# Performance work log

Measured on AMD Instinct MI355X. Metric: run time of the kernel, lower is better.

Reference implementation:

```python
import jax, jax.numpy as jnp
import numpy as np

N = 100000        # num nodes
F_IN = 256        # params['topo_feature']
C = 128           # params['num_edge'] (hidden & GCN channels)
E = 1_600_000     # num edges (avg degree 16)


def setup_inputs() -> dict:
    key = jax.random.key(0)
    k = jax.random.split(key, 6)
    x = jax.random.normal(k[0], (N, F_IN), dtype=jnp.float32)
    edge_index = jax.random.randint(k[1], (2, E), 0, N, dtype=jnp.int32)
    # fc1: Linear(F_IN, C)
    W1 = jax.random.normal(k[2], (C, F_IN), dtype=jnp.float32) * (1.0 / np.sqrt(F_IN))
    b1 = jnp.zeros((C,), dtype=jnp.float32)
    # GCNConv linear: Linear(C, C, bias=False) weight + separate bias added post-aggregation
    W2 = jax.random.normal(k[3], (C, C), dtype=jnp.float32) * (1.0 / np.sqrt(C))
    b2 = jnp.zeros((C,), dtype=jnp.float32)
    return {"x": x, "edge_index": edge_index, "W1": W1, "b1": b1, "W2": W2, "b2": b2}


def reference(x, edge_index, W1, b1, W2, b2):
    # fc1 + relu
    h = jax.nn.relu(x @ W1.T + b1)                       # [N, C]
    # GCNConv: transform, add self-loops, sym-normalize, scatter-add
    z = h @ W2.T                                         # [N, C]
    loop = jnp.arange(N, dtype=edge_index.dtype)
    src = jnp.concatenate([edge_index[0], loop])         # [E+N]
    dst = jnp.concatenate([edge_index[1], loop])         # [E+N]
    deg = jax.ops.segment_sum(jnp.ones_like(dst, jnp.float32), dst, num_segments=N)
    dinv = jnp.where(deg > 0, jax.lax.rsqrt(jnp.maximum(deg, 1.0)), 0.0)
    norm = (dinv[src] * dinv[dst])[:, None]              # [E+N, 1]
    out = jax.ops.segment_sum(z[src] * norm, dst, num_segments=N) + b2
    return out
```

## Files before the change

kernel.cpp:

```cpp
#include <hip/hip_runtime.h>

typedef unsigned short ushort;
typedef __bf16 bf16x8 __attribute__((ext_vector_type(8)));
typedef float f32x4 __attribute__((ext_vector_type(4)));

#define F_IN 256
#define CCH  128
#define BSH  7
#define BNODES 128
#define NBUCK 1024
#define CHUNK 2048

__device__ __forceinline__ ushort f2bf(float f) {
    union { float f; unsigned i; } u; u.f = f;
    unsigned r = u.i + 0x7fffu + ((u.i >> 16) & 1u);
    return (ushort)(r >> 16);
}
__device__ __forceinline__ float2 bf2f2(unsigned u) {
    union { unsigned i; float f; } lo, hi;
    lo.i = u << 16;
    hi.i = u & 0xffff0000u;
    return make_float2(lo.f, hi.f);
}
__device__ __forceinline__ void gload_lds16(const void* g, void* l) {
    __builtin_amdgcn_global_load_lds((const __attribute__((address_space(1))) unsigned*)g,
                                     (__attribute__((address_space(3))) unsigned*)l, 16, 0, 0);
}

__global__ __launch_bounds__(256)
void hist_cvt(const int* __restrict__ dst, int* __restrict__ histC, int* __restrict__ histT,
              int E, int nchunks, int ncp,
              const float* __restrict__ W1, const float* __restrict__ W2,
              ushort* __restrict__ w1b, ushort* __restrict__ w2b)
{
    const int blk = blockIdx.x, t = threadIdx.x;
    if (blk >= nchunks) {
        int i = (blk - nchunks) * 256 + t;
        if (i < CCH * F_IN) {
            int c  = i & 31;
            int cs = c ^ (((i >> 9) & 3) << 3);
            w1b[(i & ~31) | cs] = f2bf(W1[i]);
        } else {
            int j = i - CCH * F_IN;
            if (j < CCH * CCH) w2b[j] = f2bf(W2[j]);
        }
        return;
    }
    __shared__ int h[NBUCK];
    for (int i = t; i < NBUCK; i += 256) h[i] = 0;
    __syncthreads();
    int cb = blk * CHUNK, ce = min(cb + CHUNK, E);
    for (int e = cb + t; e < ce; e += 256)
        atomicAdd(&h[dst[e] >> BSH], 1);
    __syncthreads();
    const int ncp16 = ncp * 16;
    for (int i = t; i < NBUCK; i += 256) {
        int v = h[i];
        histC[blk * NBUCK + i] = v;
        histT[(i >> 4) * ncp16 + blk * 16 + (i & 15)] = v;
    }
}

__global__ __launch_bounds__(1024)
void scan_buckets(int* __restrict__ histT, int* __restrict__ btot, int nchunks, int ncp)
{
    const int w = threadIdx.x >> 6;
    const int b = blockIdx.x * 16 + w;
    const int lane = threadIdx.x & 63;
    const int tb = blockIdx.x * (ncp * 16) + w;
    int carry = 0;
    for (int c = 0; c < nchunks; c += 64) {
        int idx = c + lane;
        int v = (idx < nchunks) ? histT[tb + idx * 16] : 0;
        int inc = v;
#pragma unroll
        for (int off = 1; off < 64; off <<= 1) {
            int x = __shfl_up(inc, off, 64);
            if (lane >= off) inc += x;
        }
        if (idx < nchunks) histT[tb + idx * 16] = carry + inc - v;
        carry += __shfl(inc, 63, 64);
    }
    if (lane == 0) btot[b] = carry;
}

__device__ __forceinline__ void partition_body(unsigned* smem4,
    const int* __restrict__ src, const int* __restrict__ dst,
    const int* __restrict__ histC, const int* __restrict__ histPre,
    const int* __restrict__ btot, int* __restrict__ gbase,
    unsigned* __restrict__ pairs, int E, int ncp, int blk)
{
    int* lcur = (int*)smem4;
    int* off  = lcur + NBUCK;
    int* wsum = off + NBUCK;
    const int t = threadIdx.x;
    const int wv = t >> 6, lane = t & 63;

    int4 cv = *(const int4*)&histC[blk * NBUCK + 4 * t];
    int tsum = cv.x + cv.y + cv.z + cv.w;
    int inc = tsum;
#pragma unroll
    for (int o = 1; o < 64; o <<= 1) {
        int x = __shfl_up(inc, o, 64);
        if (lane >= o) inc += x;
    }
    if (lane == 63) wsum[wv] = inc;
    __syncthreads();
    int woff = 0;
    if (wv > 0) woff += wsum[0];
    if (wv > 1) woff += wsum[1];
    if (wv > 2) woff += wsum[2];
    int l0 = woff + inc - tsum, l1 = l0 + cv.x, l2 = l1 + cv.y, l3 = l2 + cv.z;
    lcur[4 * t] = l0; lcur[4 * t + 1] = l1; lcur[4 * t + 2] = l2; lcur[4 * t + 3] = l3;

    int4 bt = *(const int4*)&btot[4 * t];
    int bsum = bt.x + bt.y + bt.z + bt.w;
    int binc = bsum;
#pragma unroll
    for (int o = 1; o < 64; o <<= 1) {
        int x = __shfl_up(binc, o, 64);
        if (lane >= o) binc += x;
    }
    __syncthreads();
    if (lane == 63) wsum[wv] = binc;
    __syncthreads();
    int bwoff = 0;
    if (wv > 0) bwoff += wsum[0];
    if (wv > 1) bwoff += wsum[1];
    if (wv > 2) bwoff += wsum[2];
    int b0 = bwoff + binc - bsum, b1 = b0 + bt.x, b2 = b1 + bt.y, b3 = b2 + bt.z;
    if (blk == 0) {
        *(int4*)&gbase[4 * t] = make_int4(b0, b1, b2, b3);
        if (t == 255) gbase[NBUCK] = b3 + bt.w;
    }
    int4 pf = *(const int4*)&histPre[(t >> 2) * (ncp * 16) + blk * 16 + (t & 3) * 4];
    off[4 * t]     = b0 + pf.x - l0;
    off[4 * t + 1] = b1 + pf.y - l1;
    off[4 * t + 2] = b2 + pf.z - l2;
    off[4 * t + 3] = b3 + pf.w - l3;
    __syncthreads();

    const int cb = blk * CHUNK, ce = min(cb + CHUNK, E);
    for (int e = cb + t; e < ce; e += 256) {
        int d = dst[e];
        int b = d >> BSH;
        unsigned packed = ((unsigned)src[e] << BSH) | (unsigned)(d & (BNODES - 1));
        int p = atomicAdd(&lcur[b], 1);
        pairs[off[b] + p] = packed;
    }
}

__device__ __forceinline__ void csr_body(unsigned* smem4,
    const unsigned* __restrict__ pairs, const int* __restrict__ base,
    int* __restrict__ row_start, float* __restrict__ dinv,
    unsigned* __restrict__ csr, int N, int E, int b, int lastb)
{
    int* deg  = (int*)smem4;
    int* cur  = deg + BNODES;
    int* wsum = cur + BNODES;
    const int t = threadIdx.x;
    if (t < BNODES) deg[t] = 0;
    __syncthreads();
    const int rb = base[b], re = base[b + 1];
    for (int e = rb + t; e < re; e += 256)
        atomicAdd(&deg[pairs[e] & (BNODES - 1)], 1);
    __syncthreads();
    int v = (t < BNODES) ? deg[t] : 0;
    int inc = v;
#pragma unroll
    for (int o = 1; o < 64; o <<= 1) {
        int x = __shfl_up(inc, o, 64);
        if ((t & 63) >= o) inc += x;
    }
    if (t < BNODES && (t & 63) == 63) wsum[t >> 6] = inc;
    __syncthreads();
    const int n0 = b << BSH;
    if (t < BNODES) {
        int excl = inc - v + ((t >= 64) ? wsum[0] : 0);
        cur[t] = rb + excl;
        if (n0 + t < N) {
            row_start[n0 + t] = rb + excl;
            dinv[n0 + t] = rsqrtf((float)v + 1.0f);
        }
    }
    if (b == lastb && t == 0) row_start[N] = E;
    __syncthreads();
    for (int e = rb + t; e < re; e += 256) {
        unsigned p = pairs[e];
        int slot = atomicAdd(&cur[p & (BNODES - 1)], 1);
        csr[slot] = p >> BSH;
    }
}

__device__ __forceinline__ void gemm_body(unsigned* smem4,
    const float* __restrict__ X, const ushort* __restrict__ W1b,
    const ushort* __restrict__ W2b, const float* __restrict__ b1,
    ushort* __restrict__ Zq, int M, int m0)
{
    ushort* smem = (ushort*)smem4;
    ushort* Ht = smem;
    const int tid  = threadIdx.x;
    const int wave = tid >> 6, lane = tid & 63;
    const int wm = (wave & 1) * 64, wn = (wave >> 1) * 64;
    const int lr = lane & 15, lq = lane >> 4;

    const int arow = tid >> 2;
    const int aq   = tid & 3;

    float4 ar[2][2];
    auto loadX = [&](int k0) {
#pragma unroll
        for (int it = 0; it < 2; it++) {
            int grow = min(m0 + arow + it * 64, M - 1);
            const float* p = &X[(long)grow * F_IN + k0 + aq * 8];
            ar[it][0] = *(const float4*)p;
            ar[it][1] = *(const float4*)(p + 4);
        }
    };
    auto writeA = [&](ushort* As) {
#pragma unroll
        for (int it = 0; it < 2; it++) {
            int row = arow + it * 64;
            ushort u[8] = { f2bf(ar[it][0].x), f2bf(ar[it][0].y), f2bf(ar[it][0].z), f2bf(ar[it][0].w),
                            f2bf(ar[it][1].x), f2bf(ar[it][1].y), f2bf(ar[it][1].z), f2bf(ar[it][1].w) };
            *(uint4*)&As[row * 32 + ((aq ^ ((row >> 1) & 3)) << 3)] = *(uint4*)u;
        }
    };
    auto stageB = [&](int k0, ushort* Bs) {
#pragma unroll
        for (int it = 0; it < 2; it++) {
            int r0 = wave * 32 + it * 16;
            const ushort* g = &W1b[(long)(r0 + (lane >> 2)) * F_IN + k0 + (lane & 3) * 8];
            gload_lds16(g, &Bs[r0 * 32]);
        }
    };

    f32x4 acc[4][4] = {};
    loadX(0);
    stageB(0, smem + 4096);
    writeA(smem);
    __syncthreads();
    for (int k0 = 0; k0 < F_IN; k0 += 32) {
        const int cur = (k0 >> 5) & 1;
        ushort* As = smem + cur * 8192;
        ushort* Bs = As + 4096;
        const bool more = (k0 + 32 < F_IN);
        if (more) {
            stageB(k0 + 32, smem + (cur ^ 1) * 8192 + 4096);
            loadX(k0 + 32);
        }
        bf16x8 af[4], bfr[4];
#pragma unroll
        for (int t4 = 0; t4 < 4; t4++) {
            int ra = wm + t4 * 16 + lr;
            int rb = wn + t4 * 16 + lr;
            af[t4]  = *(bf16x8*)&As[ra * 32 + ((lq ^ ((ra >> 1) & 3)) << 3)];
            bfr[t4] = *(bf16x8*)&Bs[rb * 32 + ((lq ^ ((rb >> 1) & 3)) << 3)];
        }
#pragma unroll
        for (int i = 0; i < 4; i++)
#pragma unroll
            for (int j = 0; j < 4; j++)
                acc[i][j] = __builtin_amdgcn_mfma_f32_16x16x32_bf16(af[i], bfr[j], acc[i][j], 0, 0, 0);
        if (more) writeA(smem + (cur ^ 1) * 8192);
        __syncthreads();
    }

    uint4 wb[2][4];
#pragma unroll
    for (int t4 = 0; t4 < 4; t4++)
        wb[0][t4] = *(const uint4*)&W2b[(long)(wn + t4 * 16 + lr) * CCH + lq * 8];

    {
        float bv[4];
#pragma unroll
        for (int j = 0; j < 4; j++) bv[j] = b1[wn + j * 16 + lr];
#pragma unroll
        for (int i = 0; i < 4; i++)
#pragma unroll
            for (int r = 0; r < 4; r++) {
                int row = wm + i * 16 + lq * 4 + r;
                int rx  = (row & 7) << 3;
#pragma unroll
                for (int j = 0; j < 4; j++)
                    Ht[row * 128 + ((wn + j * 16 + lr) ^ rx)] = f2bf(fmaxf(acc[i][j][r] + bv[j], 0.f));
            }
    }
    __syncthreads();

    f32x4 acc2[4][4] = {};
#pragma unroll
    for (int kk = 0; kk < 4; kk++) {
        const int k0 = kk * 32;
        if (kk < 3) {
#pragma unroll
            for (int t4 = 0; t4 < 4; t4++)
                wb[(kk + 1) & 1][t4] =
                    *(const uint4*)&W2b[(long)(wn + t4 * 16 + lr) * CCH + k0 + 32 + lq * 8];
        }
        bf16x8 af[4];
#pragma unroll
        for (int t4 = 0; t4 < 4; t4++) {
            int ra = wm + t4 * 16 + lr;
            af[t4] = *(bf16x8*)&Ht[ra * 128 + ((k0 + lq * 8) ^ ((ra & 7) << 3))];
        }
#pragma unroll
        for (int i = 0; i < 4; i++)
#pragma unroll
            for (int j = 0; j < 4; j++)
                acc2[i][j] = __builtin_amdgcn_mfma_f32_16x16x32_bf16(af[i], *(bf16x8*)&wb[kk & 1][j],
                                                                     acc2[i][j], 0, 0, 0);
    }
    __syncthreads();

#pragma unroll
    for (int i = 0; i < 4; i++)
#pragma unroll
        for (int r = 0; r < 4; r++) {
            int row = wm + i * 16 + lq * 4 + r;
            int rx  = (row & 7) << 3;
#pragma unroll
            for (int j = 0; j < 4; j++)
                Ht[row * 128 + ((wn + j * 16 + lr) ^ rx)] = f2bf(acc2[i][j][r]);
        }
    __syncthreads();
    {
        int colq = tid & 15, row0 = tid >> 4;
#pragma unroll
        for (int i = 0; i < 8; i++) {
            int row = row0 + i * 16;
            if (m0 + row < M)
                *(uint4*)&Zq[(long)(m0 + row) * CCH + colq * 8] =
                    *(uint4*)&Ht[row * 128 + ((colq * 8) ^ ((row & 7) << 3))];
        }
    }
}

__global__ __launch_bounds__(256)
void u_part_gemm(const int* __restrict__ src, const int* __restrict__ dst,
                 const int* __restrict__ histC, const int* __restrict__ histPre,
                 const int* __restrict__ btot, int* __restrict__ gbase,
                 unsigned* __restrict__ pairs, int E, int ncp, int nchunks,
                 const float* __restrict__ X, const ushort* __restrict__ W1b,
                 const ushort* __restrict__ W2b, const float* __restrict__ b1,
                 ushort* __restrict__ Zq, int M)
{
    __shared__ unsigned smem4[8192];
    const int bid = blockIdx.x;
    if (bid < nchunks) {
        const int x = bid & 7, i = bid >> 3;
        const int q = nchunks >> 3, r = nchunks & 7;
        const int chunk = (x < r) ? x * (q + 1) + i : r * (q + 1) + (x - r) * q + i;
        partition_body(smem4, src, dst, histC, histPre, btot, gbase, pairs, E, ncp, chunk);
    } else {
        gemm_body(smem4, X, W1b, W2b, b1, Zq, M, (bid - nchunks) * 128);
    }
}

__global__ __launch_bounds__(256)
void u_csr_gemm(const unsigned* __restrict__ pairs, const int* __restrict__ base,
                int* __restrict__ row_start, float* __restrict__ dinv,
                unsigned* __restrict__ csr, int N, int E, int nbuck, int ngA,
                const float* __restrict__ X, const ushort* __restrict__ W1b,
                const ushort* __restrict__ W2b, const float* __restrict__ b1,
                ushort* __restrict__ Zq, int M)
{
    __shared__ unsigned smem4[8192];
    const int bid = blockIdx.x;
    if (bid < nbuck)
        csr_body(smem4, pairs, base, row_start, dinv, csr, N, E, bid, nbuck - 1);
    else
        gemm_body(smem4, X, W1b, W2b, b1, Zq, M, (ngA + bid - nbuck) * 128);
}

__global__ __launch_bounds__(256)
void gather_nodes(const unsigned* __restrict__ zq, const unsigned* __restrict__ csr,
                  const int* __restrict__ row_start, const float* __restrict__ dinv,
                  const float* __restrict__ b2, float* __restrict__ out, int N)
{
    const int node = blockIdx.x * 4 + (threadIdx.x >> 6);
    const int lane = threadIdx.x & 63;
    if (node >= N) return;

    const float di = dinv[node];
    float2 zs = bf2f2(zq[(long)node * 64 + lane]);
    float acc0 = di * zs.x, acc1 = di * zs.y;

    const int rs = row_start[node];
    const int re = row_start[node + 1];
    for (int j = rs; j < re; j += 8) {
        unsigned sI[8], zv[8];
        float dv[8];
#pragma unroll
        for (int q = 0; q < 8; q++) sI[q] = csr[min(j + q, re - 1)];
#pragma unroll
        for (int q = 0; q < 8; q++) zv[q] = zq[(long)sI[q] * 64 + lane];
#pragma unroll
        for (int q = 0; q < 8; q++) dv[q] = (j + q < re) ? dinv[sI[q]] : 0.f;
#pragma unroll
        for (int q = 0; q < 8; q++) { float2 f = bf2f2(zv[q]); acc0 += dv[q] * f.x; acc1 += dv[q] * f.y; }
    }

    float2 o;
    o.x = b2[lane * 2 + 0] + di * acc0;
    o.y = b2[lane * 2 + 1] + di * acc1;
    *(float2*)&out[(long)node * CCH + lane * 2] = o;
}

extern "C" void kernel_launch(void* const* d_in, const int* in_sizes, int n_in,
                              void* d_out, int out_size, void* d_ws, size_t ws_size,
                              hipStream_t stream)
{
    const float* x  = (const float*)d_in[0];
    const int*   ei = (const int*)d_in[1];
    const float* W1 = (const float*)d_in[2];
    const float* b1 = (const float*)d_in[3];
    const float* W2 = (const float*)d_in[4];
    const float* b2 = (const float*)d_in[5];
    float* out = (float*)d_out;

    const int N = in_sizes[0] / F_IN;
    const int E = in_sizes[1] / 2;
    const int* src = ei;
    const int* dst = ei + E;

    const int nchunks = (E + CHUNK - 1) / CHUNK;
    const int ncp     = (nchunks + 63) & ~63;
    const int nbuck   = (N + BNODES - 1) / BNODES;
    const int ngrid   = (N + 127) / 128;
    const int ngA     = (ngrid + 1) / 2;
    const int ngB     = ngrid - ngA;
    const int ncvt    = (CCH * F_IN + CCH * CCH + 255) / 256;

    char* ws = (char*)d_ws;
    ushort* zq    = (ushort*)ws;   ws += (size_t)N * CCH * 2;
    ushort* w1b   = (ushort*)ws;   ws += (size_t)CCH * F_IN * 2;
    ushort* w2b   = (ushort*)ws;   ws += (size_t)CCH * CCH * 2;
    unsigned* prs = (unsigned*)ws; ws += (size_t)E * 4;
    unsigned* csr = (unsigned*)ws; ws += (size_t)E * 4;
    int* rstart   = (int*)ws;      ws += ((size_t)N + 1) * 4;
    float* dinv   = (float*)ws;    ws += (size_t)N * 4;
    int* histC    = (int*)ws;      ws += (size_t)nchunks * NBUCK * 4;
    int* histT    = (int*)ws;      ws += (size_t)NBUCK * ncp * 4;
    int* btot     = (int*)ws;      ws += NBUCK * 4;
    int* gbase    = (int*)ws;      ws += (NBUCK + 1) * 4;

    hist_cvt<<<nchunks + ncvt, 256, 0, stream>>>(dst, histC, histT, E, nchunks, ncp, W1, W2, w1b, w2b);
    scan_buckets<<<NBUCK / 16, 1024, 0, stream>>>(histT, btot, nchunks, ncp);
    u_part_gemm<<<nchunks + ngA, 256, 0, stream>>>(src, dst, histC, histT, btot, gbase, prs,
                                                   E, ncp, nchunks, x, w1b, w2b, b1, zq, N);
    u_csr_gemm<<<nbuck + ngB, 256, 0, stream>>>(prs, gbase, rstart, dinv, csr, N, E,
                                                nbuck, ngA, x, w1b, w2b, b1, zq, N);
    gather_nodes<<<(N + 3) / 4, 256, 0, stream>>>((const unsigned*)zq, csr, rstart, dinv, b2, out, N);
}
```

Measured before the change: 308.1 us.

## Compute degrees early and fold source dinv into Z to drop per-edge gather

Per-node degrees are now counted with global atomics during the histogram pass, and dinv is computed in extra blocks of the scan kernel. The GEMM epilogue pre-scales each Z row by its own dinv, so the gather kernel no longer loads dinv[src] per edge and just sums masked bf16 rows. This removes a dependent random load per edge and the degree counting in the CSR build. In exchange it adds a memset, 1.6M global atomics, and one more bf16 rounding applied after the dinv scaling. CHUNK is also doubled, halving the histogram block count.

```diff
diff --git a/kernel.cpp b/kernel.cpp
--- a/kernel.cpp
+++ b/kernel.cpp
@@ -9,7 +9,7 @@
 #define BSH  7
 #define BNODES 128
 #define NBUCK 1024
-#define CHUNK 2048
+#define CHUNK 4096
 
 __device__ __forceinline__ ushort f2bf(float f) {
     union { float f; unsigned i; } u; u.f = f;
@@ -29,7 +29,7 @@
 
 __global__ __launch_bounds__(256)
 void hist_cvt(const int* __restrict__ dst, int* __restrict__ histC, int* __restrict__ histT,
-              int E, int nchunks, int ncp,
+              int* __restrict__ deg, int E, int nchunks, int ncp,
               const float* __restrict__ W1, const float* __restrict__ W2,
               ushort* __restrict__ w1b, ushort* __restrict__ w2b)
 {
@@ -50,8 +50,11 @@
     for (int i = t; i < NBUCK; i += 256) h[i] = 0;
     __syncthreads();
     int cb = blk * CHUNK, ce = min(cb + CHUNK, E);
-    for (int e = cb + t; e < ce; e += 256)
-        atomicAdd(&h[dst[e] >> BSH], 1);
+    for (int e = cb + t; e < ce; e += 256) {
+        int d = dst[e];
+        atomicAdd(&h[d >> BSH], 1);
+        atomicAdd(&deg[d], 1);
+    }
     __syncthreads();
     const int ncp16 = ncp * 16;
     for (int i = t; i < NBUCK; i += 256) {
@@ -62,8 +65,14 @@
 }
 
 __global__ __launch_bounds__(1024)
-void scan_buckets(int* __restrict__ histT, int* __restrict__ btot, int nchunks, int ncp)
-{
+void scan_buckets(int* __restrict__ histT, int* __restrict__ btot, int nchunks, int ncp,
+                  const int* __restrict__ deg, float* __restrict__ dinv, int N)
+{
+    if ((int)blockIdx.x >= 64) {
+        int i = (blockIdx.x - 64) * 1024 + threadIdx.x;
+        if (i < N) dinv[i] = rsqrtf((float)deg[i] + 1.0f);
+        return;
+    }
     const int w = threadIdx.x >> 6;
     const int b = blockIdx.x * 16 + w;
     const int lane = threadIdx.x & 63;
@@ -152,20 +161,15 @@
 
 __device__ __forceinline__ void csr_body(unsigned* smem4,
     const unsigned* __restrict__ pairs, const int* __restrict__ base,
-    int* __restrict__ row_start, float* __restrict__ dinv,
+    const int* __restrict__ deg, int* __restrict__ row_start,
     unsigned* __restrict__ csr, int N, int E, int b, int lastb)
 {
-    int* deg  = (int*)smem4;
-    int* cur  = deg + BNODES;
+    int* cur  = (int*)smem4;
     int* wsum = cur + BNODES;
     const int t = threadIdx.x;
-    if (t < BNODES) deg[t] = 0;
-    __syncthreads();
     const int rb = base[b], re = base[b + 1];
-    for (int e = rb + t; e < re; e += 256)
-        atomicAdd(&deg[pairs[e] & (BNODES - 1)], 1);
-    __syncthreads();
-    int v = (t < BNODES) ? deg[t] : 0;
+    const int n0 = b << BSH;
+    int v = (t < BNODES && n0 + t < N) ? deg[n0 + t] : 0;
     int inc = v;
 #pragma unroll
     for (int o = 1; o < 64; o <<= 1) {
@@ -174,14 +178,10 @@
     }
     if (t < BNODES && (t & 63) == 63) wsum[t >> 6] = inc;
     __syncthreads();
-    const int n0 = b << BSH;
     if (t < BNODES) {
         int excl = inc - v + ((t >= 64) ? wsum[0] : 0);
         cur[t] = rb + excl;
-        if (n0 + t < N) {
-            row_start[n0 + t] = rb + excl;
-            dinv[n0 + t] = rsqrtf((float)v + 1.0f);
-        }
+        if (n0 + t < N) row_start[n0 + t] = rb + excl;
     }
     if (b == lastb && t == 0) row_start[N] = E;
     __syncthreads();
@@ -195,7 +195,7 @@
 __device__ __forceinline__ void gemm_body(unsigned* smem4,
     const float* __restrict__ X, const ushort* __restrict__ W1b,
     const ushort* __restrict__ W2b, const float* __restrict__ b1,
-    ushort* __restrict__ Zq, int M, int m0)
+    const float* __restrict__ dinv, ushort* __restrict__ Zq, int M, int m0)
 {
     ushort* smem = (ushort*)smem4;
     ushort* Ht = smem;
@@ -319,9 +319,10 @@
         for (int r = 0; r < 4; r++) {
             int row = wm + i * 16 + lq * 4 + r;
             int rx  = (row & 7) << 3;
+            float di = (m0 + row < M) ? dinv[m0 + row] : 0.f;
 #pragma unroll
             for (int j = 0; j < 4; j++)
-                Ht[row * 128 + ((wn + j * 16 + lr) ^ rx)] = f2bf(acc2[i][j][r]);
+                Ht[row * 128 + ((wn + j * 16 + lr) ^ rx)] = f2bf(acc2[i][j][r] * di);
         }
     __syncthreads();
     {
@@ -343,7 +344,7 @@
                  unsigned* __restrict__ pairs, int E, int ncp, int nchunks,
                  const float* __restrict__ X, const ushort* __restrict__ W1b,
                  const ushort* __restrict__ W2b, const float* __restrict__ b1,
-                 ushort* __restrict__ Zq, int M)
+                 const float* __restrict__ dinv, ushort* __restrict__ Zq, int M)
 {
     __shared__ unsigned smem4[8192];
     const int bid = blockIdx.x;
@@ -353,24 +354,24 @@
         const int chunk = (x < r) ? x * (q + 1) + i : r * (q + 1) + (x - r) * q + i;
         partition_body(smem4, src, dst, histC, histPre, btot, gbase, pairs, E, ncp, chunk);
     } else {
-        gemm_body(smem4, X, W1b, W2b, b1, Zq, M, (bid - nchunks) * 128);
+        gemm_body(smem4, X, W1b, W2b, b1, dinv, Zq, M, (bid - nchunks) * 128);
     }
 }
 
 __global__ __launch_bounds__(256)
 void u_csr_gemm(const unsigned* __restrict__ pairs, const int* __restrict__ base,
-                int* __restrict__ row_start, float* __restrict__ dinv,
+                const int* __restrict__ deg, int* __restrict__ row_start,
                 unsigned* __restrict__ csr, int N, int E, int nbuck, int ngA,
                 const float* __restrict__ X, const ushort* __restrict__ W1b,
                 const ushort* __restrict__ W2b, const float* __restrict__ b1,
-                ushort* __restrict__ Zq, int M)
+                const float* __restrict__ dinv, ushort* __restrict__ Zq, int M)
 {
     __shared__ unsigned smem4[8192];
     const int bid = blockIdx.x;
     if (bid < nbuck)
-        csr_body(smem4, pairs, base, row_start, dinv, csr, N, E, bid, nbuck - 1);
+        csr_body(smem4, pairs, base, deg, row_start, csr, N, E, bid, nbuck - 1);
     else
-        gemm_body(smem4, X, W1b, W2b, b1, Zq, M, (ngA + bid - nbuck) * 128);
+        gemm_body(smem4, X, W1b, W2b, b1, dinv, Zq, M, (ngA + bid - nbuck) * 128);
 }
 
 __global__ __launch_bounds__(256)
@@ -383,28 +384,27 @@
     if (node >= N) return;
 
     const float di = dinv[node];
-    float2 zs = bf2f2(zq[(long)node * 64 + lane]);
-    float acc0 = di * zs.x, acc1 = di * zs.y;
+    float2 zs = bf2f2(zq[(unsigned)node * 64u + lane]);
+    float acc0 = zs.x, acc1 = zs.y;
 
     const int rs = row_start[node];
     const int re = row_start[node + 1];
     for (int j = rs; j < re; j += 8) {
-        unsigned sI[8], zv[8];
-        float dv[8];
+        unsigned sI[8], zv[8], mk[8];
 #pragma unroll
         for (int q = 0; q < 8; q++) sI[q] = csr[min(j + q, re - 1)];
 #pragma unroll
-        for (int q = 0; q < 8; q++) zv[q] = zq[(long)sI[q] * 64 + lane];
-#pragma unroll
-        for (int q = 0; q < 8; q++) dv[q] = (j + q < re) ? dinv[sI[q]] : 0.f;
-#pragma unroll
-        for (int q = 0; q < 8; q++) { float2 f = bf2f2(zv[q]); acc0 += dv[q] * f.x; acc1 += dv[q] * f.y; }
+        for (int q = 0; q < 8; q++) zv[q] = zq[sI[q] * 64u + (unsigned)lane];
+#pragma unroll
+        for (int q = 0; q < 8; q++) mk[q] = (j + q < re) ? 0xffffffffu : 0u;
+#pragma unroll
+        for (int q = 0; q < 8; q++) { float2 f = bf2f2(zv[q] & mk[q]); acc0 += f.x; acc1 += f.y; }
     }
 
     float2 o;
     o.x = b2[lane * 2 + 0] + di * acc0;
     o.y = b2[lane * 2 + 1] + di * acc1;
-    *(float2*)&out[(long)node * CCH + lane * 2] = o;
+    *(float2*)&out[(unsigned)node * (unsigned)CCH + lane * 2u] = o;
 }
 
 extern "C" void kernel_launch(void* const* d_in, const int* in_sizes, int n_in,
@@ -431,6 +431,7 @@
     const int ngA     = (ngrid + 1) / 2;
     const int ngB     = ngrid - ngA;
     const int ncvt    = (CCH * F_IN + CCH * CCH + 255) / 256;
+    const int nz      = (N + 1023) / 1024;
 
     char* ws = (char*)d_ws;
     ushort* zq    = (ushort*)ws;   ws += (size_t)N * CCH * 2;
@@ -440,16 +441,19 @@
     unsigned* csr = (unsigned*)ws; ws += (size_t)E * 4;
     int* rstart   = (int*)ws;      ws += ((size_t)N + 1) * 4;
     float* dinv   = (float*)ws;    ws += (size_t)N * 4;
+    int* deg      = (int*)ws;      ws += (size_t)N * 4;
     int* histC    = (int*)ws;      ws += (size_t)nchunks * NBUCK * 4;
     int* histT    = (int*)ws;      ws += (size_t)NBUCK * ncp * 4;
     int* btot     = (int*)ws;      ws += NBUCK * 4;
     int* gbase    = (int*)ws;      ws += (NBUCK + 1) * 4;
 
-    hist_cvt<<<nchunks + ncvt, 256, 0, stream>>>(dst, histC, histT, E, nchunks, ncp, W1, W2, w1b, w2b);
-    scan_buckets<<<NBUCK / 16, 1024, 0, stream>>>(histT, btot, nchunks, ncp);
+    hipMemsetAsync(deg, 0, (size_t)N * 4, stream);
+    hist_cvt<<<nchunks + ncvt, 256, 0, stream>>>(dst, histC, histT, deg, E, nchunks, ncp,
+                                                 W1, W2, w1b, w2b);
+    scan_buckets<<<64 + nz, 1024, 0, stream>>>(histT, btot, nchunks, ncp, deg, dinv, N);
     u_part_gemm<<<nchunks + ngA, 256, 0, stream>>>(src, dst, histC, histT, btot, gbase, prs,
-                                                   E, ncp, nchunks, x, w1b, w2b, b1, zq, N);
-    u_csr_gemm<<<nbuck + ngB, 256, 0, stream>>>(prs, gbase, rstart, dinv, csr, N, E,
-                                                nbuck, ngA, x, w1b, w2b, b1, zq, N);
+                                                   E, ncp, nchunks, x, w1b, w2b, b1, dinv, zq, N);
+    u_csr_gemm<<<nbuck + ngB, 256, 0, stream>>>(prs, gbase, deg, rstart, csr, N, E,
+                                                nbuck, ngA, x, w1b, w2b, b1, dinv, zq, N);
     gather_nodes<<<(N + 3) / 4, 256, 0, stream>>>((const unsigned*)zq, csr, rstart, dinv, b2, out, N);
 }
```

Measured after the change: 364.7 us. 1.18x slower.
